# Kernel tuning notes

Measured on AMD Instinct MI355X. Metric: run time of the kernel, lower is better.

## Reference

```python
import jax, jax.numpy as jnp
import numpy as np

B, C, H, W = 1, 448, 64, 64
K, M, PAD, STRIDE = 7, 7, 3, 1
CG = C // K          # key/query channels (KeyQueryMap divides by k) = 64
GP_HID = int(0.5 * CG)  # geometry prior hidden channels = 32
K2 = K * K
CENTER = K2 // 2


def conv1x1(x, w, b):
    # x: (B, Cin, H, W), w: (Cout, Cin), b: (Cout,)
    return jnp.einsum('bchw,oc->bohw', x, w) + b[None, :, None, None]


def unfold(x):
    # torch.nn.Unfold(K, dilation=1, padding=PAD, stride=STRIDE)
    # output layout: (B, Cin*K2, L) with dim1 index = c*K2 + (di*K + dj)
    Bc, Cc, Hc, Wc = x.shape
    xp = jnp.pad(x, ((0, 0), (0, 0), (PAD, PAD), (PAD, PAD)))
    Ho = (Hc + 2 * PAD - K) // STRIDE + 1
    Wo = (Wc + 2 * PAD - K) // STRIDE + 1
    patches = [xp[:, :, di:di + Ho * STRIDE:STRIDE, dj:dj + Wo * STRIDE:STRIDE]
               for di in range(K) for dj in range(K)]
    u = jnp.stack(patches, axis=2)  # (B, Cc, K2, Ho, Wo)
    return u.reshape(Bc, Cc * K2, Ho * Wo), Ho, Wo


def geometry_prior(gp_w1, gp_b1, gp_w2, gp_b2):
    ar = jnp.arange(-(K // 2), K // 2 + 1, dtype=jnp.float32)   # -3..3
    x_pos = jnp.broadcast_to(ar[None, :], (K, K))
    y_pos = jnp.broadcast_to(ar[::-1][:, None], (K, K))          # 3..-3 down rows
    pos = jnp.stack([x_pos, y_pos], axis=0)[None]                # (1, 2, K, K)
    h = jax.nn.relu(conv1x1(pos, gp_w1, gp_b1))
    out = conv1x1(h, gp_w2, gp_b2)                               # (1, CG, K, K)
    return out.reshape(1, CG, 1, K2)


def setup_inputs() -> dict:
    key = jax.random.key(0)
    ks = jax.random.split(key, 12)
    def lin(k, cout, cin):
        return jax.random.normal(k, (cout, cin), jnp.float32) / np.sqrt(cin)
    inp = {
        'x': jax.random.normal(ks[0], (B, C, H, W), jnp.float32),
        'Wk': lin(ks[1], CG, C), 'bk': jnp.zeros((CG,), jnp.float32),
        'Wq': lin(ks[2], CG, C), 'bq': jnp.zeros((CG,), jnp.float32),
        'gp_w1': lin(ks[3], GP_HID, 2), 'gp_b1': jax.random.normal(ks[4], (GP_HID,), jnp.float32) * 0.01,
        'gp_w2': lin(ks[5], CG, GP_HID), 'gp_b2': jax.random.normal(ks[6], (CG,), jnp.float32) * 0.01,
        'Wf': lin(ks[7], C, C), 'bf': jnp.zeros((C,), jnp.float32),
    }
    return inp


def reference(x, Wk, bk, Wq, bq, gp_w1, gp_b1, gp_w2, gp_b2, Wf, bf):
    gpk = geometry_prior(gp_w1, gp_b1, gp_w2, gp_b2)        # (1, CG, 1, K2)
    km = conv1x1(x, Wk, bk)                                  # (B, CG, H, W)
    qm = conv1x1(x, Wq, bq)
    ku, Ho, Wo = unfold(km)
    L = Ho * Wo
    ku = ku.reshape(B, CG, L, K2)   # same row-major semantics as torch .view
    qu, _, _ = unfold(qm)
    qu = qu.reshape(B, CG, L, K2)
    ak = ku * qu[:, :, :, CENTER:CENTER + 1]                 # (B, CG, L, K2)
    ck = jax.nn.softmax(ak + gpk, axis=-1)                   # (B, CG, L, K2)
    xu, _, _ = unfold(x)
    xu = xu.reshape(B, M, C // M, L, K2)                     # (B, M, CG, L, K2)
    # ck broadcasts over the M axis (valid since B == 1); sum over window dim
    pre = jnp.einsum('bglp,bmglp->bmgl', ck, xu).reshape(B, C, Ho, Wo)
    return conv1x1(pre, Wf, bf)
```

## Files before the change

### kernel.cpp

```cpp
#include <hip/hip_runtime.h>
#include <hip/hip_bf16.h>

#define CC   448
#define CGC  64
#define MMM  7
#define HWSZ 4096
#define KK2  49
#define GPH  32

typedef __attribute__((ext_vector_type(8))) short   short8;
typedef __attribute__((ext_vector_type(4))) float   f32x4;
typedef __attribute__((ext_vector_type(4))) unsigned short us4;

__device__ __forceinline__ unsigned short f2b(float f) {
    union { __hip_bfloat16 h; unsigned short u; } cv;
    cv.h = __float2bfloat16(f);
    return cv.u;
}

__global__ __launch_bounds__(256) void kq_mfma(
    const float* __restrict__ x,
    const float* __restrict__ Wk, const float* __restrict__ bk,
    const float* __restrict__ Wq, const float* __restrict__ bq,
    float* __restrict__ km, float* __restrict__ qm)
{
    __shared__ unsigned short As[4096];
    __shared__ unsigned short Bs[512];

    const int tid  = threadIdx.x;
    const int nT   = blockIdx.x * 16;
    const int lane = tid & 63;
    const int wid  = tid >> 6;
    const int wm   = wid * 32;
    const int l15  = lane & 15;
    const int l4   = lane >> 4;

    const int ar  = tid >> 3;
    const int ak  = tid & 7;
    const int bkr = tid >> 3;
    const int bn2 = tid & 7;

    f32x4 acc[2];
    acc[0] = (f32x4){0.f, 0.f, 0.f, 0.f};
    acc[1] = (f32x4){0.f, 0.f, 0.f, 0.f};

    float4 a0 = *(const float4*)(Wk + (size_t)ar * CC + ak * 4);
    float4 a1 = *(const float4*)(Wk + (size_t)(ar + 32) * CC + ak * 4);
    float4 a2 = *(const float4*)(Wq + (size_t)ar * CC + ak * 4);
    float4 a3 = *(const float4*)(Wq + (size_t)(ar + 32) * CC + ak * 4);
    float2 b0 = *(const float2*)(x + (size_t)bkr * HWSZ + nT + bn2 * 2);

    for (int kt = 0; kt < 14; ++kt) {
        {
            int kg = ak >> 1, jo = (ak & 1) * 4;
            us4 w;
            w = (us4){ f2b(a0.x), f2b(a0.y), f2b(a0.z), f2b(a0.w) };
            *(us4*)&As[kg * 1024 + (ar +  0) * 8 + jo] = w;
            w = (us4){ f2b(a1.x), f2b(a1.y), f2b(a1.z), f2b(a1.w) };
            *(us4*)&As[kg * 1024 + (ar + 32) * 8 + jo] = w;
            w = (us4){ f2b(a2.x), f2b(a2.y), f2b(a2.z), f2b(a2.w) };
            *(us4*)&As[kg * 1024 + (ar + 64) * 8 + jo] = w;
            w = (us4){ f2b(a3.x), f2b(a3.y), f2b(a3.z), f2b(a3.w) };
            *(us4*)&As[kg * 1024 + (ar + 96) * 8 + jo] = w;
            int base = (bkr >> 3) * 128 + bn2 * 16 + (bkr & 7);
            Bs[base]     = f2b(b0.x);
            Bs[base + 8] = f2b(b0.y);
        }
        __syncthreads();
        if (kt < 13) {
            int ko = (kt + 1) * 32;
            a0 = *(const float4*)(Wk + (size_t)ar * CC + ko + ak * 4);
            a1 = *(const float4*)(Wk + (size_t)(ar + 32) * CC + ko + ak * 4);
            a2 = *(const float4*)(Wq + (size_t)ar * CC + ko + ak * 4);
            a3 = *(const float4*)(Wq + (size_t)(ar + 32) * CC + ko + ak * 4);
            b0 = *(const float2*)(x + (size_t)(ko + bkr) * HWSZ + nT + bn2 * 2);
        }
        short8 fa0 = *(short8*)&As[l4 * 1024 + (wm + l15) * 8];
        short8 fa1 = *(short8*)&As[l4 * 1024 + (wm + 16 + l15) * 8];
        short8 fb0 = *(short8*)&Bs[l4 * 128 + l15 * 8];
        acc[0] = __builtin_amdgcn_mfma_f32_16x16x32_bf16(fa0, fb0, acc[0], 0, 0, 0);
        acc[1] = __builtin_amdgcn_mfma_f32_16x16x32_bf16(fa1, fb0, acc[1], 0, 0, 0);
        __syncthreads();
    }
    const bool isK = (wid < 2);
    float*       Cd   = isK ? km : qm;
    const float* bias = isK ? bk : bq;
    const int rbase = wm & 63;
    #pragma unroll
    for (int wm2 = 0; wm2 < 2; ++wm2)
        #pragma unroll
        for (int r = 0; r < 4; ++r) {
            int row = rbase + wm2 * 16 + l4 * 4 + r;
            int col = nT + l15;
            Cd[(size_t)row * HWSZ + col] = acc[wm2][r] + bias[row];
        }
}

__global__ __launch_bounds__(256) void fconv_mfma(
    const float* __restrict__ pre,
    const float* __restrict__ Wf, const float* __restrict__ bfv,
    float* __restrict__ out)
{
    __shared__ unsigned short As[2048];
    __shared__ unsigned short Bs[1024];

    const int tid  = threadIdx.x;
    const int nT   = blockIdx.x * 32;
    const int oT   = blockIdx.y * 64;
    const int lane = tid & 63;
    const int wid  = tid >> 6;
    const int l15  = lane & 15;
    const int l4   = lane >> 4;

    const int ar  = tid >> 3;
    const int ak  = tid & 7;
    const int bkr = tid >> 3;
    const int bn4 = tid & 7;

    const float* __restrict__ A = Wf + (size_t)oT * CC;

    f32x4 acc[2];
    acc[0] = (f32x4){0.f, 0.f, 0.f, 0.f};
    acc[1] = (f32x4){0.f, 0.f, 0.f, 0.f};

    float4 a0 = *(const float4*)(A + (size_t)ar * CC + ak * 4);
    float4 a1 = *(const float4*)(A + (size_t)(ar + 32) * CC + ak * 4);
    float4 b0 = *(const float4*)(pre + (size_t)bkr * HWSZ + nT + bn4 * 4);

    for (int kt = 0; kt < 14; ++kt) {
        {
            int kg = ak >> 1, jo = (ak & 1) * 4;
            us4 w;
            w = (us4){ f2b(a0.x), f2b(a0.y), f2b(a0.z), f2b(a0.w) };
            *(us4*)&As[kg * 512 + (ar +  0) * 8 + jo] = w;
            w = (us4){ f2b(a1.x), f2b(a1.y), f2b(a1.z), f2b(a1.w) };
            *(us4*)&As[kg * 512 + (ar + 32) * 8 + jo] = w;
            int base = (bkr >> 3) * 256 + bn4 * 32 + (bkr & 7);
            Bs[base]      = f2b(b0.x);
            Bs[base + 8]  = f2b(b0.y);
            Bs[base + 16] = f2b(b0.z);
            Bs[base + 24] = f2b(b0.w);
        }
        __syncthreads();
        if (kt < 13) {
            int ko = (kt + 1) * 32;
            a0 = *(const float4*)(A + (size_t)ar * CC + ko + ak * 4);
            a1 = *(const float4*)(A + (size_t)(ar + 32) * CC + ko + ak * 4);
            b0 = *(const float4*)(pre + (size_t)(ko + bkr) * HWSZ + nT + bn4 * 4);
        }
        short8 fa  = *(short8*)&As[l4 * 512 + (wid * 16 + l15) * 8];
        short8 fb0 = *(short8*)&Bs[l4 * 256 + l15 * 8];
        short8 fb1 = *(short8*)&Bs[l4 * 256 + (16 + l15) * 8];
        acc[0] = __builtin_amdgcn_mfma_f32_16x16x32_bf16(fa, fb0, acc[0], 0, 0, 0);
        acc[1] = __builtin_amdgcn_mfma_f32_16x16x32_bf16(fa, fb1, acc[1], 0, 0, 0);
        __syncthreads();
    }
    #pragma unroll
    for (int wn2 = 0; wn2 < 2; ++wn2)
        #pragma unroll
        for (int r = 0; r < 4; ++r) {
            int row = oT + wid * 16 + l4 * 4 + r;
            int col = nT + wn2 * 16 + l15;
            out[(size_t)row * HWSZ + col] = acc[wn2][r] + bfv[row];
        }
}

#define GLO 196
#define GHI 260
#define PGW (GLO + HWSZ + GHI)
#define NPG 8

__global__ __launch_bounds__(1024, 4) void attn_kernel(
    const float* __restrict__ km, const float* __restrict__ qm,
    const float* __restrict__ x,
    const float* __restrict__ gw1, const float* __restrict__ gb1,
    const float* __restrict__ gw2, const float* __restrict__ gb2,
    float* __restrict__ pre)
{
    __shared__ __align__(16) float sm[NPG * PGW];
    __shared__ float gpk_s[KK2];

    const int tid = threadIdx.x;
    const int g   = blockIdx.y;
    const int lp  = blockIdx.x * 1024 + tid;

    if (tid < NPG * 114) {
        int page = tid / 114;
        int r    = tid - page * 114;
        int w    = (r < 49) ? r * 4 : (GLO + HWSZ + (r - 49) * 4);
        *(float4*)&sm[page * PGW + w] = (float4){0.f, 0.f, 0.f, 0.f};
    }
    {
        const float4* s0 = (const float4*)(km + (size_t)g * HWSZ);
        *(float4*)&sm[GLO + tid * 4] = s0[tid];
        #pragma unroll
        for (int m = 0; m < MMM; ++m) {
            const float4* sx = (const float4*)(x + (size_t)(m * CGC + g) * HWSZ);
            *(float4*)&sm[(m + 1) * PGW + GLO + tid * 4] = sx[tid];
        }
    }
    if (tid < KK2) {
        int di = tid / 7, dj = tid - di * 7;
        float xp = (float)(dj - 3);
        float yp = (float)(3 - di);
        float a2 = gb2[g];
        #pragma unroll
        for (int j = 0; j < GPH; ++j) {
            float h = fmaxf(gw1[j * 2 + 0] * xp + gw1[j * 2 + 1] * yp + gb1[j], 0.f);
            a2 = fmaf(gw2[g * GPH + j], h, a2);
        }
        gpk_s[tid] = a2;
    }

    float qc;
    {
        int nc = lp * KK2 + 24;
        int pc = nc >> 12, lc = nc & 4095;
        int dic = (pc * 37) >> 8, djc = pc - dic * 7;
        int i = (lc >> 6) + dic - 3, j = (lc & 63) + djc - 3;
        bool ok = ((unsigned)i < 64u) && ((unsigned)j < 64u);
        qc = ok ? qm[(size_t)g * HWSZ + i * 64 + j] : 0.f;
    }

    const int n0 = lp * KK2;
    const int p0 = n0 >> 12;
    const int l0 = n0 & 4095;
    const int ts = ((p0 + 1) << 12) - n0;
    const int di0 = (p0 * 37) >> 8, dj0 = p0 - di0 * 7;
    const int p1  = p0 + 1;
    const int di1 = (p1 * 37) >> 8, dj1 = p1 - di1 * 7;
    const int dm0 = dj0 - 3, dm1 = dj1 - 3;
    const int B0 = GLO + l0 + (di0 - 3) * 64 + dm0;
    const int B1 = GLO + l0 - HWSZ + (di1 - 3) * 64 + dm1;
    const int c0 = l0 + (dm0 > 0 ? dm0 : 0), w0 = (dm0 < 0) ? -dm0 : dm0;
    const int c1 = l0 + (dm1 > 0 ? dm1 : 0), w1 = (dm1 < 0) ? -dm1 : dm1;

    __syncthreads();

    float d = 0.f;
    float acc[MMM];
    #pragma unroll
    for (int m = 0; m < MMM; ++m) acc[m] = 0.f;

    #pragma unroll
    for (int tp = 0; tp < 24; ++tp) {
        const int t0 = 2 * tp, t1 = t0 + 1;
        const bool s1 = (t1 >= ts);
        const int bb = s1 ? B1 : B0;
        const int cc = s1 ? c1 : c0;
        const int ww = s1 ? w1 : w0;
        float kv0 = sm[bb + t0];
        float kv1 = sm[bb + t1];
        const bool bad0 = (((cc + t0) & 63) < ww);
        const bool bad1 = (((cc + t1) & 63) < ww);
        kv0 = bad0 ? 0.f : kv0;
        kv1 = bad1 ? 0.f : kv1;
        const float e0 = __expf(fmaf(kv0, qc, gpk_s[t0]));
        const float e1 = __expf(fmaf(kv1, qc, gpk_s[t1]));
        d += e0 + e1;
        const float em0 = bad0 ? 0.f : e0;
        const float em1 = bad1 ? 0.f : e1;
        #pragma unroll
        for (int m = 0; m < MMM; ++m) {
            const int ob = bb + (m + 1) * PGW;
            acc[m] = fmaf(em1, sm[ob + t1], fmaf(em0, sm[ob + t0], acc[m]));
        }
    }
    {
        const bool s1 = (48 >= ts);
        const int bb = s1 ? B1 : B0;
        const int cc = s1 ? c1 : c0;
        const int ww = s1 ? w1 : w0;
        float kv = sm[bb + 48];
        const bool bad = (((cc + 48) & 63) < ww);
        kv = bad ? 0.f : kv;
        const float e = __expf(fmaf(kv, qc, gpk_s[48]));
        d += e;
        const float em = bad ? 0.f : e;
        #pragma unroll
        for (int m = 0; m < MMM; ++m)
            acc[m] = fmaf(em, sm[bb + (m + 1) * PGW + 48], acc[m]);
    }
    if (ts < 49 && (ts & 1)) {
        const int tw = ts - 1;
        const float gw = gpk_s[tw];
        float kw = sm[B1 + tw];
        const bool bw = (((c1 + tw) & 63) < w1);
        kw = bw ? 0.f : kw;
        const float ew  = __expf(fmaf(kw, qc, gw));
        const float emw = bw ? 0.f : ew;
        float kr = sm[B0 + tw];
        const bool br = (((c0 + tw) & 63) < w0);
        kr = br ? 0.f : kr;
        const float er  = __expf(fmaf(kr, qc, gw));
        const float emr = br ? 0.f : er;
        d += er - ew;
        #pragma unroll
        for (int m = 0; m < MMM; ++m)
            acc[m] += emr * sm[B0 + (m + 1) * PGW + tw]
                    - emw * sm[B1 + (m + 1) * PGW + tw];
    }

    const float inv = 1.f / d;
    #pragma unroll
    for (int m = 0; m < MMM; ++m)
        pre[(size_t)(m * CGC + g) * HWSZ + lp] = acc[m] * inv;
}

extern "C" void kernel_launch(void* const* d_in, const int* in_sizes, int n_in,
                              void* d_out, int out_size, void* d_ws, size_t ws_size,
                              hipStream_t stream) {
    const float* x   = (const float*)d_in[0];
    const float* Wk  = (const float*)d_in[1];
    const float* bk  = (const float*)d_in[2];
    const float* Wq  = (const float*)d_in[3];
    const float* bq  = (const float*)d_in[4];
    const float* gw1 = (const float*)d_in[5];
    const float* gb1 = (const float*)d_in[6];
    const float* gw2 = (const float*)d_in[7];
    const float* gb2 = (const float*)d_in[8];
    const float* Wf  = (const float*)d_in[9];
    const float* bfv = (const float*)d_in[10];
    float* out = (float*)d_out;

    float* km  = (float*)d_ws;
    float* qm  = km + CGC * HWSZ;
    float* pre = qm + CGC * HWSZ;

    kq_mfma    <<<dim3(256),    256, 0, stream>>>(x, Wk, bk, Wq, bq, km, qm);
    attn_kernel<<<dim3(4, CGC), 1024, 0, stream>>>(km, qm, x, gw1, gb1, gw2, gb2, pre);
    fconv_mfma <<<dim3(128, 7), 256, 0, stream>>>(pre, Wf, bfv, out);
}
```

Measured before the change: 114.1 us.

## Stage full K-dimension in LDS for both 1x1-conv GEMMs with 1024-thread blocks

Both MFMA GEMM kernels (key/query projection and final 1x1 conv) now load the whole 448-deep K dimension of their A and B tiles into shared memory in one pass, instead of a 14-step double-buffered loop with two barriers per step. kq_mfma splits K across two wave groups and reduces the partial sums through LDS. fconv_mfma gets larger 112x64 output tiles per block. The aim is to remove per-step barrier and latency overhead, but the large LDS footprint (about 120-156 KB per block) limits residency to one block per CU and gives no load/compute overlap.

```diff
diff --git a/kernel.cpp b/kernel.cpp
--- a/kernel.cpp
+++ b/kernel.cpp
@@ -18,151 +18,146 @@
     return cv.u;
 }
 
-__global__ __launch_bounds__(256) void kq_mfma(
+__global__ __launch_bounds__(1024, 4) void kq_mfma(
     const float* __restrict__ x,
     const float* __restrict__ Wk, const float* __restrict__ bk,
     const float* __restrict__ Wq, const float* __restrict__ bq,
     float* __restrict__ km, float* __restrict__ qm)
 {
-    __shared__ unsigned short As[4096];
-    __shared__ unsigned short Bs[512];
+    __shared__ unsigned short As[57344];
+    __shared__ unsigned short Bs[7168];
+    __shared__ float         red[2048];
 
     const int tid  = threadIdx.x;
     const int nT   = blockIdx.x * 16;
     const int lane = tid & 63;
     const int wid  = tid >> 6;
-    const int wm   = wid * 32;
     const int l15  = lane & 15;
     const int l4   = lane >> 4;
 
-    const int ar  = tid >> 3;
-    const int ak  = tid & 7;
-    const int bkr = tid >> 3;
-    const int bn2 = tid & 7;
-
-    f32x4 acc[2];
-    acc[0] = (f32x4){0.f, 0.f, 0.f, 0.f};
-    acc[1] = (f32x4){0.f, 0.f, 0.f, 0.f};
-
-    float4 a0 = *(const float4*)(Wk + (size_t)ar * CC + ak * 4);
-    float4 a1 = *(const float4*)(Wk + (size_t)(ar + 32) * CC + ak * 4);
-    float4 a2 = *(const float4*)(Wq + (size_t)ar * CC + ak * 4);
-    float4 a3 = *(const float4*)(Wq + (size_t)(ar + 32) * CC + ak * 4);
-    float2 b0 = *(const float2*)(x + (size_t)bkr * HWSZ + nT + bn2 * 2);
-
-    for (int kt = 0; kt < 14; ++kt) {
-        {
-            int kg = ak >> 1, jo = (ak & 1) * 4;
-            us4 w;
-            w = (us4){ f2b(a0.x), f2b(a0.y), f2b(a0.z), f2b(a0.w) };
-            *(us4*)&As[kg * 1024 + (ar +  0) * 8 + jo] = w;
-            w = (us4){ f2b(a1.x), f2b(a1.y), f2b(a1.z), f2b(a1.w) };
-            *(us4*)&As[kg * 1024 + (ar + 32) * 8 + jo] = w;
-            w = (us4){ f2b(a2.x), f2b(a2.y), f2b(a2.z), f2b(a2.w) };
-            *(us4*)&As[kg * 1024 + (ar + 64) * 8 + jo] = w;
-            w = (us4){ f2b(a3.x), f2b(a3.y), f2b(a3.z), f2b(a3.w) };
-            *(us4*)&As[kg * 1024 + (ar + 96) * 8 + jo] = w;
-            int base = (bkr >> 3) * 128 + bn2 * 16 + (bkr & 7);
-            Bs[base]     = f2b(b0.x);
-            Bs[base + 8] = f2b(b0.y);
-        }
-        __syncthreads();
-        if (kt < 13) {
-            int ko = (kt + 1) * 32;
-            a0 = *(const float4*)(Wk + (size_t)ar * CC + ko + ak * 4);
-            a1 = *(const float4*)(Wk + (size_t)(ar + 32) * CC + ko + ak * 4);
-            a2 = *(const float4*)(Wq + (size_t)ar * CC + ko + ak * 4);
-            a3 = *(const float4*)(Wq + (size_t)(ar + 32) * CC + ko + ak * 4);
-            b0 = *(const float2*)(x + (size_t)(ko + bkr) * HWSZ + nT + bn2 * 2);
-        }
-        short8 fa0 = *(short8*)&As[l4 * 1024 + (wm + l15) * 8];
-        short8 fa1 = *(short8*)&As[l4 * 1024 + (wm + 16 + l15) * 8];
-        short8 fb0 = *(short8*)&Bs[l4 * 128 + l15 * 8];
-        acc[0] = __builtin_amdgcn_mfma_f32_16x16x32_bf16(fa0, fb0, acc[0], 0, 0, 0);
-        acc[1] = __builtin_amdgcn_mfma_f32_16x16x32_bf16(fa1, fb0, acc[1], 0, 0, 0);
-        __syncthreads();
-    }
-    const bool isK = (wid < 2);
-    float*       Cd   = isK ? km : qm;
-    const float* bias = isK ? bk : bq;
-    const int rbase = wm & 63;
-    #pragma unroll
-    for (int wm2 = 0; wm2 < 2; ++wm2)
+    #pragma unroll
+    for (int i = 0; i < 14; ++i) {
+        int idx = tid + i * 1024;
+        int row = idx / 112;
+        int c   = idx - row * 112;
+        const float* src = (row < 64) ? (Wk + (size_t)row * CC)
+                                      : (Wq + (size_t)(row - 64) * CC);
+        float4 v = *(const float4*)(src + c * 4);
+        int kg = c >> 1, jo = (c & 1) * 4;
+        *(us4*)&As[kg * 1024 + row * 8 + jo] =
+            (us4){ f2b(v.x), f2b(v.y), f2b(v.z), f2b(v.w) };
+    }
+    #pragma unroll
+    for (int i = 0; i < 2; ++i) {
+        int idx = tid + i * 1024;
+        if (idx < 1792) {
+            int row = idx >> 2, c4 = idx & 3;
+            float4 v = *(const float4*)(x + (size_t)row * HWSZ + nT + c4 * 4);
+            int kg = row >> 3, j = row & 7;
+            int b  = kg * 128 + c4 * 32 + j;
+            Bs[b]      = f2b(v.x);
+            Bs[b + 8]  = f2b(v.y);
+            Bs[b + 16] = f2b(v.z);
+            Bs[b + 24] = f2b(v.w);
+        }
+    }
+    __syncthreads();
+
+    const int mt = (wid & 7) * 16;
+    const int kh = wid >> 3;
+    f32x4 acc = (f32x4){0.f, 0.f, 0.f, 0.f};
+    #pragma unroll
+    for (int i = 0; i < 7; ++i) {
+        int K4 = kh * 28 + i * 4;
+        short8 fa = *(short8*)&As[(K4 + l4) * 1024 + (mt + l15) * 8];
+        short8 fb = *(short8*)&Bs[(K4 + l4) * 128 + l15 * 8];
+        acc = __builtin_amdgcn_mfma_f32_16x16x32_bf16(fa, fb, acc, 0, 0, 0);
+    }
+    if (kh == 1)
+        *(f32x4*)&red[(wid & 7) * 256 + lane * 4] = acc;
+    __syncthreads();
+    if (kh == 0) {
+        f32x4 o = *(f32x4*)&red[(wid & 7) * 256 + lane * 4];
+        const bool isK = (mt < 64);
+        float*       Cd   = isK ? km : qm;
+        const float* bias = isK ? bk : bq;
+        const int rb = (mt & 63) + l4 * 4;
         #pragma unroll
         for (int r = 0; r < 4; ++r) {
-            int row = rbase + wm2 * 16 + l4 * 4 + r;
-            int col = nT + l15;
-            Cd[(size_t)row * HWSZ + col] = acc[wm2][r] + bias[row];
-        }
-}
-
-__global__ __launch_bounds__(256) void fconv_mfma(
+            int row = rb + r;
+            Cd[(size_t)row * HWSZ + nT + l15] = acc[r] + o[r] + bias[row];
+        }
+    }
+}
+
+__global__ __launch_bounds__(1024, 4) void fconv_mfma(
     const float* __restrict__ pre,
     const float* __restrict__ Wf, const float* __restrict__ bfv,
     float* __restrict__ out)
 {
-    __shared__ unsigned short As[2048];
-    __shared__ unsigned short Bs[1024];
+    __shared__ unsigned short As[50176];
+    __shared__ unsigned short Bs[28672];
 
     const int tid  = threadIdx.x;
-    const int nT   = blockIdx.x * 32;
-    const int oT   = blockIdx.y * 64;
+    const int bid  = blockIdx.x;
+    const int nT   = (bid >> 2) * 64;
+    const int oT   = (bid & 3) * 112;
     const int lane = tid & 63;
     const int wid  = tid >> 6;
     const int l15  = lane & 15;
     const int l4   = lane >> 4;
 
-    const int ar  = tid >> 3;
-    const int ak  = tid & 7;
-    const int bkr = tid >> 3;
-    const int bn4 = tid & 7;
-
-    const float* __restrict__ A = Wf + (size_t)oT * CC;
-
-    f32x4 acc[2];
-    acc[0] = (f32x4){0.f, 0.f, 0.f, 0.f};
-    acc[1] = (f32x4){0.f, 0.f, 0.f, 0.f};
-
-    float4 a0 = *(const float4*)(A + (size_t)ar * CC + ak * 4);
-    float4 a1 = *(const float4*)(A + (size_t)(ar + 32) * CC + ak * 4);
-    float4 b0 = *(const float4*)(pre + (size_t)bkr * HWSZ + nT + bn4 * 4);
-
-    for (int kt = 0; kt < 14; ++kt) {
-        {
-            int kg = ak >> 1, jo = (ak & 1) * 4;
-            us4 w;
-            w = (us4){ f2b(a0.x), f2b(a0.y), f2b(a0.z), f2b(a0.w) };
-            *(us4*)&As[kg * 512 + (ar +  0) * 8 + jo] = w;
-            w = (us4){ f2b(a1.x), f2b(a1.y), f2b(a1.z), f2b(a1.w) };
-            *(us4*)&As[kg * 512 + (ar + 32) * 8 + jo] = w;
-            int base = (bkr >> 3) * 256 + bn4 * 32 + (bkr & 7);
-            Bs[base]      = f2b(b0.x);
-            Bs[base + 8]  = f2b(b0.y);
-            Bs[base + 16] = f2b(b0.z);
-            Bs[base + 24] = f2b(b0.w);
-        }
-        __syncthreads();
-        if (kt < 13) {
-            int ko = (kt + 1) * 32;
-            a0 = *(const float4*)(A + (size_t)ar * CC + ko + ak * 4);
-            a1 = *(const float4*)(A + (size_t)(ar + 32) * CC + ko + ak * 4);
-            b0 = *(const float4*)(pre + (size_t)(ko + bkr) * HWSZ + nT + bn4 * 4);
-        }
-        short8 fa  = *(short8*)&As[l4 * 512 + (wid * 16 + l15) * 8];
-        short8 fb0 = *(short8*)&Bs[l4 * 256 + l15 * 8];
-        short8 fb1 = *(short8*)&Bs[l4 * 256 + (16 + l15) * 8];
-        acc[0] = __builtin_amdgcn_mfma_f32_16x16x32_bf16(fa, fb0, acc[0], 0, 0, 0);
-        acc[1] = __builtin_amdgcn_mfma_f32_16x16x32_bf16(fa, fb1, acc[1], 0, 0, 0);
-        __syncthreads();
-    }
-    #pragma unroll
-    for (int wn2 = 0; wn2 < 2; ++wn2)
-        #pragma unroll
-        for (int r = 0; r < 4; ++r) {
-            int row = oT + wid * 16 + l4 * 4 + r;
-            int col = nT + wn2 * 16 + l15;
-            out[(size_t)row * HWSZ + col] = acc[wn2][r] + bfv[row];
-        }
+    #pragma unroll
+    for (int i = 0; i < 13; ++i) {
+        int idx = tid + i * 1024;
+        if (idx < 12544) {
+            int row = idx / 112;
+            int c   = idx - row * 112;
+            float4 v = *(const float4*)(Wf + (size_t)(oT + row) * CC + c * 4);
+            int kg = c >> 1, jo = (c & 1) * 4;
+            *(us4*)&As[kg * 896 + row * 8 + jo] =
+                (us4){ f2b(v.x), f2b(v.y), f2b(v.z), f2b(v.w) };
+        }
+    }
+    #pragma unroll
+    for (int i = 0; i < 7; ++i) {
+        int idx = tid + i * 1024;
+        int row = idx >> 4, c4 = idx & 15;
+        float4 v = *(const float4*)(pre + (size_t)row * HWSZ + nT + c4 * 4);
+        int kg = row >> 3, j = row & 7;
+        int b  = kg * 512 + c4 * 32 + j;
+        Bs[b]      = f2b(v.x);
+        Bs[b + 8]  = f2b(v.y);
+        Bs[b + 16] = f2b(v.z);
+        Bs[b + 24] = f2b(v.w);
+    }
+    __syncthreads();
+
+    if (wid < 14) {
+        const int mt = (wid % 7) * 16;
+        const int np = wid / 7;
+        f32x4 a0 = (f32x4){0.f, 0.f, 0.f, 0.f};
+        f32x4 a1 = (f32x4){0.f, 0.f, 0.f, 0.f};
+        #pragma unroll
+        for (int i = 0; i < 14; ++i) {
+            int K4 = i * 4;
+            short8 fa  = *(short8*)&As[(K4 + l4) * 896 + (mt + l15) * 8];
+            short8 fb0 = *(short8*)&Bs[(K4 + l4) * 512 + (np * 32 + l15) * 8];
+            short8 fb1 = *(short8*)&Bs[(K4 + l4) * 512 + (np * 32 + 16 + l15) * 8];
+            a0 = __builtin_amdgcn_mfma_f32_16x16x32_bf16(fa, fb0, a0, 0, 0, 0);
+            a1 = __builtin_amdgcn_mfma_f32_16x16x32_bf16(fa, fb1, a1, 0, 0, 0);
+        }
+        #pragma unroll
+        for (int wn2 = 0; wn2 < 2; ++wn2) {
+            const f32x4 a = wn2 ? a1 : a0;
+            #pragma unroll
+            for (int r = 0; r < 4; ++r) {
+                int row = oT + mt + l4 * 4 + r;
+                int col = nT + np * 32 + wn2 * 16 + l15;
+                out[(size_t)row * HWSZ + col] = a[r] + bfv[row];
+            }
+        }
+    }
 }
 
 #define GLO 196
@@ -327,7 +322,7 @@
     float* qm  = km + CGC * HWSZ;
     float* pre = qm + CGC * HWSZ;
 
-    kq_mfma    <<<dim3(256),    256, 0, stream>>>(x, Wk, bk, Wq, bq, km, qm);
+    kq_mfma    <<<dim3(256),    1024, 0, stream>>>(x, Wk, bk, Wq, bq, km, qm);
     attn_kernel<<<dim3(4, CGC), 1024, 0, stream>>>(km, qm, x, gw1, gb1, gw2, gb2, pre);
-    fconv_mfma <<<dim3(128, 7), 256, 0, stream>>>(pre, Wf, bfv, out);
-}
+    fconv_mfma <<<dim3(256),    1024, 0, stream>>>(pre, Wf, bfv, out);
+}
```

Result: faster. 108.0 us (-5.3%).
